# Optimization experiments

Measured on AMD Instinct MI355X. Metric: run time of the kernel, lower is better.

The kernel has to match this reference:

```python
import jax, jax.numpy as jnp
import numpy as np

N_NODES = 20000
N_EDGES = 320000
IN_DIM = 512
HID = 256
N_GRAPHS = 256


def setup_inputs() -> dict:
    key = jax.random.key(0)
    ks = jax.random.split(key, 7)
    x = jax.random.normal(ks[0], (N_NODES, IN_DIM), dtype=jnp.float32)
    edge_index = jax.random.randint(ks[1], (2, N_EDGES), 0, N_NODES, dtype=jnp.int64)
    batch = jnp.sort(jax.random.randint(ks[2], (N_NODES,), 0, N_GRAPHS, dtype=jnp.int64))
    W = jax.random.normal(ks[3], (IN_DIM, HID), dtype=jnp.float32) * (1.0 / np.sqrt(IN_DIM))
    b = jax.random.normal(ks[4], (HID,), dtype=jnp.float32) * 0.02
    lin_w = jax.random.normal(ks[5], (HID, 1), dtype=jnp.float32) * (1.0 / np.sqrt(HID))
    lin_b = jax.random.normal(ks[6], (1,), dtype=jnp.float32) * 0.02
    return {"x": x, "edge_index": edge_index, "batch": batch,
            "W": W, "b": b, "lin_w": lin_w, "lin_b": lin_b}


def reference(x, edge_index, batch, W, b, lin_w, lin_b):
    N = x.shape[0]
    # --- GCNConv: add self-loops, symmetric normalization ---
    loop = jnp.arange(N, dtype=edge_index.dtype)
    src = jnp.concatenate([edge_index[0], loop])   # [E+N]
    dst = jnp.concatenate([edge_index[1], loop])   # [E+N]
    deg = jax.ops.segment_sum(jnp.ones_like(dst, dtype=x.dtype), dst, num_segments=N)
    dinv = jnp.where(deg > 0, jax.lax.rsqrt(deg), 0.0)          # [N]
    norm = dinv[src] * dinv[dst]                                 # [E+N]
    h = x @ W                                                    # [N, HID] dense GEMM
    msgs = h[src] * norm[:, None]                                # gather + scale
    agg = jax.ops.segment_sum(msgs, dst, num_segments=N) + b     # scatter-add
    xr = jax.nn.relu(agg)                                        # [N, HID]
    # --- global_mean_pool over graph ids ---
    sums = jax.ops.segment_sum(xr, batch, num_segments=N_GRAPHS)             # [G, HID]
    counts = jax.ops.segment_sum(jnp.ones((N,), dtype=x.dtype), batch, num_segments=N_GRAPHS)
    pooled = sums / jnp.maximum(counts, 1.0)[:, None]
    # --- linear head + sigmoid ---
    out = jax.nn.sigmoid(pooled @ lin_w + lin_b)                 # [G, 1]
    return out.reshape(-1)
```

## Files before the change

### kernel.cpp

```cpp
#include <hip/hip_runtime.h>
#include <hip/hip_bf16.h>
#include <cstdint>

typedef __attribute__((ext_vector_type(8))) _Float16 half8;
typedef __attribute__((ext_vector_type(4))) _Float16 half4;
typedef __attribute__((ext_vector_type(2))) float f32x2;
typedef __attribute__((ext_vector_type(4))) float f32x4;

#define N_NODES 20000
#define N_EDGES 320000
#define IN_DIM 512
#define HID 256
#define N_GRAPHS 256
#define NPB 8
#define DSTRIDE 64

#define PREP_WBLK 16
#define PREP_BBLK ((N_NODES + 255) / 256)
__global__ __launch_bounds__(256) void prep_kernel(const float* __restrict__ W,
                                                   const int* __restrict__ batch,
                                                   _Float16* __restrict__ wt,
                                                   int* __restrict__ counts) {
    int b = blockIdx.x, t = threadIdx.x;
    if (b < PREP_WBLK) {
        __shared__ _Float16 tile[32 * 256];
        int k0 = b * 32;
        const float4* wp = reinterpret_cast<const float4*>(W + (size_t)k0 * HID);
#pragma unroll
        for (int i = 0; i < 8; ++i) {
            float4 v = wp[i * 256 + t];
            int flat = (i * 256 + t) * 4;
            int kk = flat >> 8, n = flat & 255;
            half4 hv;
            hv[0] = (_Float16)v.x; hv[1] = (_Float16)v.y;
            hv[2] = (_Float16)v.z; hv[3] = (_Float16)v.w;
            *reinterpret_cast<half4*>(&tile[kk * 256 + n]) = hv;
        }
        __syncthreads();
        alignas(16) _Float16 vals[32];
#pragma unroll
        for (int kk = 0; kk < 32; ++kk) vals[kk] = tile[kk * 256 + t];
        uint4* op = reinterpret_cast<uint4*>((char*)wt + (size_t)t * 1024 + (size_t)k0 * 2);
        const uint4* vp = reinterpret_cast<const uint4*>(vals);
#pragma unroll
        for (int j = 0; j < 4; ++j) op[j] = vp[j];
    } else {
        int i = (b - PREP_WBLK) * 256 + t;
        if (i < N_NODES) atomicAdd(&counts[batch[i]], 1);
    }
}

#define GEMM_BLOCKS ((N_NODES + 63) / 64)
#define CSR_BLOCKS  (N_EDGES / 256)

#define LOADA(Sa, Sb, Sc, Sd, k0) do { const float* ap_ = aptr + (k0); \
    Sa = *reinterpret_cast<const float4*>(ap_);         \
    Sb = *reinterpret_cast<const float4*>(ap_ + 4);     \
    Sc = *reinterpret_cast<const float4*>(ap_ + 32);    \
    Sd = *reinterpret_cast<const float4*>(ap_ + 36); } while (0)

#define PACKA(Sa, Sb, Sc, Sd) do { \
    a0[0]=(_Float16)Sa.x; a0[1]=(_Float16)Sa.y; a0[2]=(_Float16)Sa.z; a0[3]=(_Float16)Sa.w; \
    a0[4]=(_Float16)Sb.x; a0[5]=(_Float16)Sb.y; a0[6]=(_Float16)Sb.z; a0[7]=(_Float16)Sb.w; \
    a1[0]=(_Float16)Sc.x; a1[1]=(_Float16)Sc.y; a1[2]=(_Float16)Sc.z; a1[3]=(_Float16)Sc.w; \
    a1[4]=(_Float16)Sd.x; a1[5]=(_Float16)Sd.y; a1[6]=(_Float16)Sd.z; a1[7]=(_Float16)Sd.w; } while (0)

#define LOADB(s) do { const uint4* ws_ = wsrc + 8 * (s); \
    wb0=ws_[0]; wb1=ws_[1]; wb2=ws_[2]; wb3=ws_[3];      \
    wb4=ws_[4]; wb5=ws_[5]; wb6=ws_[6]; wb7=ws_[7]; } while (0)

#define STAGEB(q) do { uint4* d_ = reinterpret_cast<uint4*>(myst + ((q) << 15)); \
    d_[0^tsw]=wb0; d_[1^tsw]=wb1; d_[2^tsw]=wb2; d_[3^tsw]=wb3;                  \
    d_[4^tsw]=wb4; d_[5^tsw]=wb5; d_[6^tsw]=wb6; d_[7^tsw]=wb7; } while (0)

#define KBARRIER() do { asm volatile("s_waitcnt lgkmcnt(0)" ::: "memory"); \
    __builtin_amdgcn_s_barrier(); asm volatile("" ::: "memory"); } while (0)

#define MFMASTEP(q) do { const char* rb_ = (const char*)bsl + ((q) << 15); \
    _Pragma("unroll")                                                      \
    for (int nt = 0; nt < 16; ++nt) {                                      \
        int c_ = nt * 16 + col; int cs_ = c_ & 7;                          \
        half8 bb0_ = *reinterpret_cast<const half8*>(rb_ + c_ * 128 + ((quad ^ cs_) << 4));       \
        acc[nt] = __builtin_amdgcn_mfma_f32_16x16x32_f16(a0, bb0_, acc[nt], 0, 0, 0);             \
        half8 bb1_ = *reinterpret_cast<const half8*>(rb_ + c_ * 128 + (((4 + quad) ^ cs_) << 4)); \
        acc[nt] = __builtin_amdgcn_mfma_f32_16x16x32_f16(a1, bb1_, acc[nt], 0, 0, 0);             \
    } } while (0)

__global__ __launch_bounds__(256, 2) void gemm_csr_kernel(const float* __restrict__ x,
                                                          const _Float16* __restrict__ wt,
                                                          unsigned char* __restrict__ h8,
                                                          const int* __restrict__ src,
                                                          const int* __restrict__ dst,
                                                          int* __restrict__ cnt2,
                                                          int* __restrict__ csr) {
    __shared__ _Float16 bsl[2 * 256 * 64];
    if (blockIdx.x >= GEMM_BLOCKS) {
        int e = (blockIdx.x - GEMM_BLOCKS) * 256 + threadIdx.x;
        int d = dst[e];
        int slot = atomicAdd(&cnt2[d], 1);
        if (slot < DSTRIDE) csr[d * DSTRIDE + slot] = src[e];
        return;
    }
    const int K = IN_DIM;
    int t    = threadIdx.x;
    int lane = t & 63;
    int wave = t >> 6;
    int col  = lane & 15;
    int quad = lane >> 4;
    int row0 = blockIdx.x * 64 + wave * 16;

    f32x4 acc[16];
#pragma unroll
    for (int i = 0; i < 16; ++i) acc[i] = (f32x4){0.f, 0.f, 0.f, 0.f};

    int arow = row0 + col;
    if (arow >= N_NODES) arow = N_NODES - 1;
    const float* aptr = x + (size_t)arow * K + quad * 8;
    const uint4* wsrc = reinterpret_cast<const uint4*>(wt + (size_t)t * K);

    char* myst = (char*)bsl + t * 128;
    int tsw = t & 7;

    float4 sA0, sA1, sA2, sA3;
    float4 sB0, sB1, sB2, sB3;
    uint4  wb0, wb1, wb2, wb3, wb4, wb5, wb6, wb7;
    half8  a0, a1;

    LOADB(0);
    LOADA(sA0, sA1, sA2, sA3, 0);
    LOADA(sB0, sB1, sB2, sB3, 64);
    STAGEB(0);
    LOADB(1);
    KBARRIER();

#pragma unroll
    for (int it = 0; it < 4; ++it) {
        PACKA(sA0, sA1, sA2, sA3);
        if (it < 3) LOADA(sA0, sA1, sA2, sA3, (2 * it + 2) * 64);
        STAGEB(1);
        if (it < 3) LOADB(2 * it + 2);
        MFMASTEP(0);
        KBARRIER();
        PACKA(sB0, sB1, sB2, sB3);
        if (it < 3) LOADA(sB0, sB1, sB2, sB3, (2 * it + 3) * 64);
        if (it < 3) { STAGEB(0); LOADB(2 * it + 3); }
        MFMASTEP(1);
        KBARRIER();
    }

    int orow0 = row0 + quad * 4;
#pragma unroll
    for (int nt = 0; nt < 16; ++nt) {
#pragma unroll
        for (int r = 0; r < 4; ++r) {
            int rr = orow0 + r;
            if (rr < N_NODES) {
                float v = acc[nt][r];
                int pk = __builtin_amdgcn_cvt_pk_fp8_f32(v, v, 0, false);
                h8[(size_t)rr * HID + nt * 16 + col] = (unsigned char)(pk & 0xff);
            }
        }
    }
}

__global__ __launch_bounds__(256, 8) void aggregate_kernel(const unsigned char* __restrict__ h8,
                                                           const float* __restrict__ bias,
                                                           const int* __restrict__ cnt2,
                                                           const int* __restrict__ csr,
                                                           const int* __restrict__ batch,
                                                           float* __restrict__ sums) {
    __shared__ float pool[NPB * HID];
    int v0  = blockIdx.x * NPB;
    int t   = threadIdx.x;
    int grp = t >> 6;
    int fl  = t & 63;
    int vg  = v0 + grp * 2;
    const float4 bf = *reinterpret_cast<const float4*>(bias + 4 * fl);

    float a0[2], a1[2], a2[2], a3[2], dvv[2];
#pragma unroll
    for (int i = 0; i < 2; ++i) {
        int v = vg + i;
        int ctrue = cnt2[v];
        int cnt = ctrue; if (cnt > DSTRIDE) cnt = DSTRIDE;
        float dv = rsqrtf((float)ctrue + 1.f);
        dvv[i] = dv;
        unsigned int u = *reinterpret_cast<const unsigned int*>(h8 + (size_t)v * HID + 4 * fl);
        f32x2 lo = __builtin_amdgcn_cvt_pk_f32_fp8(u, false);
        f32x2 hi = __builtin_amdgcn_cvt_pk_f32_fp8(u, true);
        float x0 = dv * lo[0], x1 = dv * lo[1], x2 = dv * hi[0], x3 = dv * hi[1];
        int ecv = csr[v * DSTRIDE + fl];
        int j = 0;
        for (; j + 4 <= cnt; j += 4) {
            int s0 = __shfl(ecv, j, 64);
            int s1 = __shfl(ecv, j + 1, 64);
            int s2 = __shfl(ecv, j + 2, 64);
            int s3 = __shfl(ecv, j + 3, 64);
            int c0 = cnt2[s0], c1 = cnt2[s1], c2 = cnt2[s2], c3 = cnt2[s3];
            unsigned int u0 = *reinterpret_cast<const unsigned int*>(h8 + (size_t)s0 * HID + 4 * fl);
            unsigned int u1 = *reinterpret_cast<const unsigned int*>(h8 + (size_t)s1 * HID + 4 * fl);
            unsigned int u2 = *reinterpret_cast<const unsigned int*>(h8 + (size_t)s2 * HID + 4 * fl);
            unsigned int u3 = *reinterpret_cast<const unsigned int*>(h8 + (size_t)s3 * HID + 4 * fl);
            float d0 = rsqrtf((float)c0 + 1.f);
            float d1 = rsqrtf((float)c1 + 1.f);
            float d2 = rsqrtf((float)c2 + 1.f);
            float d3 = rsqrtf((float)c3 + 1.f);
            f32x2 p;
            p = __builtin_amdgcn_cvt_pk_f32_fp8(u0, false); x0 += d0 * p[0]; x1 += d0 * p[1];
            p = __builtin_amdgcn_cvt_pk_f32_fp8(u0, true);  x2 += d0 * p[0]; x3 += d0 * p[1];
            p = __builtin_amdgcn_cvt_pk_f32_fp8(u1, false); x0 += d1 * p[0]; x1 += d1 * p[1];
            p = __builtin_amdgcn_cvt_pk_f32_fp8(u1, true);  x2 += d1 * p[0]; x3 += d1 * p[1];
            p = __builtin_amdgcn_cvt_pk_f32_fp8(u2, false); x0 += d2 * p[0]; x1 += d2 * p[1];
            p = __builtin_amdgcn_cvt_pk_f32_fp8(u2, true);  x2 += d2 * p[0]; x3 += d2 * p[1];
            p = __builtin_amdgcn_cvt_pk_f32_fp8(u3, false); x0 += d3 * p[0]; x1 += d3 * p[1];
            p = __builtin_amdgcn_cvt_pk_f32_fp8(u3, true);  x2 += d3 * p[0]; x3 += d3 * p[1];
        }
        for (; j < cnt; ++j) {
            int s = __shfl(ecv, j, 64);
            int c = cnt2[s];
            unsigned int u4 = *reinterpret_cast<const unsigned int*>(h8 + (size_t)s * HID + 4 * fl);
            float ds = rsqrtf((float)c + 1.f);
            f32x2 p;
            p = __builtin_amdgcn_cvt_pk_f32_fp8(u4, false); x0 += ds * p[0]; x1 += ds * p[1];
            p = __builtin_amdgcn_cvt_pk_f32_fp8(u4, true);  x2 += ds * p[0]; x3 += ds * p[1];
        }
        a0[i] = x0; a1[i] = x1; a2[i] = x2; a3[i] = x3;
    }

#pragma unroll
    for (int i = 0; i < 2; ++i) {
        f32x4 r;
        r[0] = fmaxf(dvv[i] * a0[i] + bf.x, 0.f);
        r[1] = fmaxf(dvv[i] * a1[i] + bf.y, 0.f);
        r[2] = fmaxf(dvv[i] * a2[i] + bf.z, 0.f);
        r[3] = fmaxf(dvv[i] * a3[i] + bf.w, 0.f);
        *reinterpret_cast<f32x4*>(&pool[(grp * 2 + i) * HID + 4 * fl]) = r;
    }
    __syncthreads();

    float acc = 0.f;
    int cur_g = batch[v0];
#pragma unroll
    for (int i = 0; i < NPB; ++i) {
        float val = pool[i * HID + t];
        int g = batch[v0 + i];
        if (g != cur_g) {
            atomicAdd(&sums[(size_t)cur_g * HID + t], acc);
            acc = 0.f;
            cur_g = g;
        }
        acc += val;
    }
    atomicAdd(&sums[(size_t)cur_g * HID + t], acc);
}

__global__ __launch_bounds__(256) void head_kernel(const float* __restrict__ sums,
                                                   const int* __restrict__ counts,
                                                   const float* __restrict__ lin_w,
                                                   const float* __restrict__ lin_b,
                                                   float* __restrict__ out) {
    int g = blockIdx.x;
    int f = threadIdx.x;
    float c = (float)counts[g];
    if (c < 1.f) c = 1.f;
    float v = (sums[(size_t)g * HID + f] / c) * lin_w[f];
#pragma unroll
    for (int off = 32; off >= 1; off >>= 1) v += __shfl_down(v, off, 64);
    __shared__ float red[4];
    if ((f & 63) == 0) red[f >> 6] = v;
    __syncthreads();
    if (f == 0) {
        float s = red[0] + red[1] + red[2] + red[3] + lin_b[0];
        out[g] = 1.0f / (1.0f + expf(-s));
    }
}

extern "C" void kernel_launch(void* const* d_in, const int* in_sizes, int n_in,
                              void* d_out, int out_size, void* d_ws, size_t ws_size,
                              hipStream_t stream) {
    const float* x     = (const float*)d_in[0];
    const int*   edge  = (const int*)d_in[1];
    const int*   batch = (const int*)d_in[2];
    const float* W     = (const float*)d_in[3];
    const float* b     = (const float*)d_in[4];
    const float* lin_w = (const float*)d_in[5];
    const float* lin_b = (const float*)d_in[6];
    float*       out   = (float*)d_out;

    const int N = N_NODES, E = N_EDGES, G = N_GRAPHS, K = IN_DIM, H = HID;
    const int* src = edge;
    const int* dst = edge + E;

    char* p = (char*)d_ws;
    auto alloc = [&](size_t bytes) {
        char* r = p;
        p += (bytes + 255) & ~(size_t)255;
        return r;
    };
    _Float16*      wt  = (_Float16*)alloc((size_t)H * K * 2);
    unsigned char* h8  = (unsigned char*)alloc((size_t)N * H);
    int*           csr = (int*)alloc((size_t)N * DSTRIDE * 4);
    char* z0 = p;
    int*   cnt2   = (int*)alloc((size_t)N * 4);
    float* sums   = (float*)alloc((size_t)G * H * 4);
    int*   counts = (int*)alloc((size_t)G * 4);
    size_t zbytes = (size_t)(p - z0);

    hipMemsetAsync(z0, 0, zbytes, stream);

    prep_kernel<<<PREP_WBLK + PREP_BBLK, 256, 0, stream>>>(W, batch, wt, counts);
    gemm_csr_kernel<<<GEMM_BLOCKS + CSR_BLOCKS, 256, 0, stream>>>(x, wt, h8, src, dst,
                                                                  cnt2, csr);
    aggregate_kernel<<<N / NPB, 256, 0, stream>>>(h8, b, cnt2, csr, batch, sums);
    head_kernel<<<G, 256, 0, stream>>>(sums, counts, lin_w, lin_b, out);
}
```

Before: 160.7 us.

## Gather four neighbors per wave with 16-byte loads and cross-lane reduction

Changes the aggregate kernel so each wave splits its lanes into four groups that each process a different neighbor per iteration, loading 16 fp8 features per lane as a uint4 instead of 4 bytes. Partial sums are combined across the groups with xor shuffles, and each lane then selects its 4-feature slice to add the self-loop term, bias and ReLU. This is meant to raise memory-level parallelism and load width for the irregular gathers, at the cost of more accumulator registers, padding work when the degree is not a multiple of four, and a shuffle reduction. The launch bound's minimum-occupancy hint drops from 8 to 6 to leave room for the extra registers.

```diff
diff --git a/kernel.cpp b/kernel.cpp
--- a/kernel.cpp
+++ b/kernel.cpp
@@ -163,78 +163,74 @@
     }
 }
 
-__global__ __launch_bounds__(256, 8) void aggregate_kernel(const unsigned char* __restrict__ h8,
+__global__ __launch_bounds__(256, 6) void aggregate_kernel(const unsigned char* __restrict__ h8,
                                                            const float* __restrict__ bias,
                                                            const int* __restrict__ cnt2,
                                                            const int* __restrict__ csr,
                                                            const int* __restrict__ batch,
                                                            float* __restrict__ sums) {
     __shared__ float pool[NPB * HID];
-    int v0  = blockIdx.x * NPB;
-    int t   = threadIdx.x;
-    int grp = t >> 6;
-    int fl  = t & 63;
-    int vg  = v0 + grp * 2;
-    const float4 bf = *reinterpret_cast<const float4*>(bias + 4 * fl);
-
-    float a0[2], a1[2], a2[2], a3[2], dvv[2];
+    int v0   = blockIdx.x * NPB;
+    int t    = threadIdx.x;
+    int wv   = t >> 6;
+    int lane = t & 63;
+    int g    = lane >> 4;
+    int k    = lane & 15;
+    int f0   = k * 16 + g * 4;
+
 #pragma unroll
     for (int i = 0; i < 2; ++i) {
-        int v = vg + i;
+        int v = v0 + wv * 2 + i;
         int ctrue = cnt2[v];
-        int cnt = ctrue; if (cnt > DSTRIDE) cnt = DSTRIDE;
+        int cnt = ctrue > DSTRIDE ? DSTRIDE : ctrue;
         float dv = rsqrtf((float)ctrue + 1.f);
-        dvv[i] = dv;
-        unsigned int u = *reinterpret_cast<const unsigned int*>(h8 + (size_t)v * HID + 4 * fl);
-        f32x2 lo = __builtin_amdgcn_cvt_pk_f32_fp8(u, false);
-        f32x2 hi = __builtin_amdgcn_cvt_pk_f32_fp8(u, true);
-        float x0 = dv * lo[0], x1 = dv * lo[1], x2 = dv * hi[0], x3 = dv * hi[1];
-        int ecv = csr[v * DSTRIDE + fl];
-        int j = 0;
-        for (; j + 4 <= cnt; j += 4) {
-            int s0 = __shfl(ecv, j, 64);
-            int s1 = __shfl(ecv, j + 1, 64);
-            int s2 = __shfl(ecv, j + 2, 64);
-            int s3 = __shfl(ecv, j + 3, 64);
-            int c0 = cnt2[s0], c1 = cnt2[s1], c2 = cnt2[s2], c3 = cnt2[s3];
-            unsigned int u0 = *reinterpret_cast<const unsigned int*>(h8 + (size_t)s0 * HID + 4 * fl);
-            unsigned int u1 = *reinterpret_cast<const unsigned int*>(h8 + (size_t)s1 * HID + 4 * fl);
-            unsigned int u2 = *reinterpret_cast<const unsigned int*>(h8 + (size_t)s2 * HID + 4 * fl);
-            unsigned int u3 = *reinterpret_cast<const unsigned int*>(h8 + (size_t)s3 * HID + 4 * fl);
-            float d0 = rsqrtf((float)c0 + 1.f);
-            float d1 = rsqrtf((float)c1 + 1.f);
-            float d2 = rsqrtf((float)c2 + 1.f);
-            float d3 = rsqrtf((float)c3 + 1.f);
+        int ecv = csr[v * DSTRIDE + lane];
+
+        f32x4 accA = {0.f, 0.f, 0.f, 0.f};
+        f32x4 accB = {0.f, 0.f, 0.f, 0.f};
+        f32x4 accC = {0.f, 0.f, 0.f, 0.f};
+        f32x4 accD = {0.f, 0.f, 0.f, 0.f};
+#pragma unroll 2
+        for (int j = 0; j < cnt; j += 4) {
+            int idx = j + g;
+            int e = __shfl(ecv, idx, 64);
+            float w = 0.f;
+            if (idx < cnt) {
+                w = rsqrtf((float)cnt2[e] + 1.f);
+            } else {
+                e = v;
+            }
+            uint4 u = *reinterpret_cast<const uint4*>(h8 + (size_t)e * HID + k * 16);
             f32x2 p;
-            p = __builtin_amdgcn_cvt_pk_f32_fp8(u0, false); x0 += d0 * p[0]; x1 += d0 * p[1];
-            p = __builtin_amdgcn_cvt_pk_f32_fp8(u0, true);  x2 += d0 * p[0]; x3 += d0 * p[1];
-            p = __builtin_amdgcn_cvt_pk_f32_fp8(u1, false); x0 += d1 * p[0]; x1 += d1 * p[1];
-            p = __builtin_amdgcn_cvt_pk_f32_fp8(u1, true);  x2 += d1 * p[0]; x3 += d1 * p[1];
-            p = __builtin_amdgcn_cvt_pk_f32_fp8(u2, false); x0 += d2 * p[0]; x1 += d2 * p[1];
-            p = __builtin_amdgcn_cvt_pk_f32_fp8(u2, true);  x2 += d2 * p[0]; x3 += d2 * p[1];
-            p = __builtin_amdgcn_cvt_pk_f32_fp8(u3, false); x0 += d3 * p[0]; x1 += d3 * p[1];
-            p = __builtin_amdgcn_cvt_pk_f32_fp8(u3, true);  x2 += d3 * p[0]; x3 += d3 * p[1];
-        }
-        for (; j < cnt; ++j) {
-            int s = __shfl(ecv, j, 64);
-            int c = cnt2[s];
-            unsigned int u4 = *reinterpret_cast<const unsigned int*>(h8 + (size_t)s * HID + 4 * fl);
-            float ds = rsqrtf((float)c + 1.f);
-            f32x2 p;
-            p = __builtin_amdgcn_cvt_pk_f32_fp8(u4, false); x0 += ds * p[0]; x1 += ds * p[1];
-            p = __builtin_amdgcn_cvt_pk_f32_fp8(u4, true);  x2 += ds * p[0]; x3 += ds * p[1];
-        }
-        a0[i] = x0; a1[i] = x1; a2[i] = x2; a3[i] = x3;
-    }
-
-#pragma unroll
-    for (int i = 0; i < 2; ++i) {
+            p = __builtin_amdgcn_cvt_pk_f32_fp8(u.x, false); accA[0] += w*p[0]; accA[1] += w*p[1];
+            p = __builtin_amdgcn_cvt_pk_f32_fp8(u.x, true);  accA[2] += w*p[0]; accA[3] += w*p[1];
+            p = __builtin_amdgcn_cvt_pk_f32_fp8(u.y, false); accB[0] += w*p[0]; accB[1] += w*p[1];
+            p = __builtin_amdgcn_cvt_pk_f32_fp8(u.y, true);  accB[2] += w*p[0]; accB[3] += w*p[1];
+            p = __builtin_amdgcn_cvt_pk_f32_fp8(u.z, false); accC[0] += w*p[0]; accC[1] += w*p[1];
+            p = __builtin_amdgcn_cvt_pk_f32_fp8(u.z, true);  accC[2] += w*p[0]; accC[3] += w*p[1];
+            p = __builtin_amdgcn_cvt_pk_f32_fp8(u.w, false); accD[0] += w*p[0]; accD[1] += w*p[1];
+            p = __builtin_amdgcn_cvt_pk_f32_fp8(u.w, true);  accD[2] += w*p[0]; accD[3] += w*p[1];
+        }
+#pragma unroll
+        for (int c = 0; c < 4; ++c) {
+            accA[c] += __shfl_xor(accA[c], 16, 64); accA[c] += __shfl_xor(accA[c], 32, 64);
+            accB[c] += __shfl_xor(accB[c], 16, 64); accB[c] += __shfl_xor(accB[c], 32, 64);
+            accC[c] += __shfl_xor(accC[c], 16, 64); accC[c] += __shfl_xor(accC[c], 32, 64);
+            accD[c] += __shfl_xor(accD[c], 16, 64); accD[c] += __shfl_xor(accD[c], 32, 64);
+        }
+        f32x4 sel = (g == 0) ? accA : (g == 1) ? accB : (g == 2) ? accC : accD;
+        unsigned int su = *reinterpret_cast<const unsigned int*>(h8 + (size_t)v * HID + f0);
+        f32x2 s0 = __builtin_amdgcn_cvt_pk_f32_fp8(su, false);
+        f32x2 s1 = __builtin_amdgcn_cvt_pk_f32_fp8(su, true);
+        sel[0] += dv * s0[0]; sel[1] += dv * s0[1];
+        sel[2] += dv * s1[0]; sel[3] += dv * s1[1];
+        const float4 bf = *reinterpret_cast<const float4*>(bias + f0);
         f32x4 r;
-        r[0] = fmaxf(dvv[i] * a0[i] + bf.x, 0.f);
-        r[1] = fmaxf(dvv[i] * a1[i] + bf.y, 0.f);
-        r[2] = fmaxf(dvv[i] * a2[i] + bf.z, 0.f);
-        r[3] = fmaxf(dvv[i] * a3[i] + bf.w, 0.f);
-        *reinterpret_cast<f32x4*>(&pool[(grp * 2 + i) * HID + 4 * fl]) = r;
+        r[0] = fmaxf(dv * sel[0] + bf.x, 0.f);
+        r[1] = fmaxf(dv * sel[1] + bf.y, 0.f);
+        r[2] = fmaxf(dv * sel[2] + bf.z, 0.f);
+        r[3] = fmaxf(dv * sel[3] + bf.w, 0.f);
+        *reinterpret_cast<f32x4*>(&pool[(wv * 2 + i) * HID + f0]) = r;
     }
     __syncthreads();
 
@@ -243,11 +239,11 @@
 #pragma unroll
     for (int i = 0; i < NPB; ++i) {
         float val = pool[i * HID + t];
-        int g = batch[v0 + i];
-        if (g != cur_g) {
+        int gg = batch[v0 + i];
+        if (gg != cur_g) {
             atomicAdd(&sums[(size_t)cur_g * HID + t], acc);
             acc = 0.f;
-            cur_g = g;
+            cur_g = gg;
         }
         acc += val;
     }
```

Result: no change. 162.9 us (+1.4%).
